# Kernel tuning notes

Measured on AMD Instinct MI355X. Metric: run time of the kernel, lower is better.

The kernel has to match this reference:

```python
import jax, jax.numpy as jnp
import numpy as np

N_NODES = 50000
N_EDGES = 800000
D_IN = 256
D_HID = 128


def setup_inputs() -> dict:
    key = jax.random.key(0)
    ks = jax.random.split(key, 10)
    x = jax.random.normal(ks[0], (N_NODES, D_IN), dtype=jnp.float32)
    edge_index = jax.random.randint(ks[1], (2, N_EDGES), 0, N_NODES, dtype=jnp.int64)
    # GCNConv params (glorot-ish init), 3 layers: 256->128, 128->128, 128->128
    def glorot(k, fan_in, fan_out):
        s = jnp.sqrt(6.0 / (fan_in + fan_out))
        return jax.random.uniform(k, (fan_in, fan_out), jnp.float32, -s, s)
    W0 = glorot(ks[2], D_IN, D_HID)
    b0 = jnp.zeros((D_HID,), jnp.float32)
    W1 = glorot(ks[3], D_HID, D_HID)
    b1 = jnp.zeros((D_HID,), jnp.float32)
    W2 = glorot(ks[4], D_HID, D_HID)
    b2 = jnp.zeros((D_HID,), jnp.float32)
    return {"x": x, "edge_index": edge_index, "W0": W0, "b0": b0,
            "W1": W1, "b1": b1, "W2": W2, "b2": b2}


def _gcn_conv(x, W, b, src, dst, deg_inv_sqrt, deg_inv):
    # PyG GCNConv: x' = D^{-1/2} (A + I) D^{-1/2} (x W) + b
    h = x @ W  # [N, d_out]
    norm = deg_inv_sqrt[src] * deg_inv_sqrt[dst]  # [E]
    msg = h[src] * norm[:, None]  # gather + scale, [E, d_out]
    agg = jax.ops.segment_sum(msg, dst, num_segments=x.shape[0])
    # self-loop contribution: norm = deg^{-1/2} * deg^{-1/2} = 1/deg
    return agg + h * deg_inv[:, None] + b


def reference(x, edge_index, W0, b0, W1, b1, W2, b2):
    src, dst = edge_index[0], edge_index[1]
    n = x.shape[0]
    # degree with self loops (computed on destination, source_to_target flow)
    deg = jax.ops.segment_sum(jnp.ones((src.shape[0],), x.dtype), dst,
                              num_segments=n) + 1.0
    deg_inv_sqrt = deg ** -0.5
    deg_inv = 1.0 / deg
    h = jax.nn.relu(_gcn_conv(x, W0, b0, src, dst, deg_inv_sqrt, deg_inv))
    h = jax.nn.relu(_gcn_conv(h, W1, b1, src, dst, deg_inv_sqrt, deg_inv))
    h = jax.nn.relu(_gcn_conv(h, W2, b2, src, dst, deg_inv_sqrt, deg_inv))
    return h
```

## Files before the change

### kernel.cpp

```cpp
#include <hip/hip_runtime.h>

#define N_NODES 50000
#define N_EDGES 800000
#define D_HID   128

typedef unsigned int uint;
typedef unsigned short ushort;
typedef __attribute__((ext_vector_type(8))) short short8;
typedef __attribute__((ext_vector_type(4))) float f32x4;

#define SCAN_NB ((N_NODES + 255) / 256)

__global__ void deg_count_k(const int* __restrict__ dst, int* __restrict__ cnt, int e) {
    int i = blockIdx.x * 256 + threadIdx.x;
    if (i < e) atomicAdd(&cnt[dst[i]], 1);
}

__global__ void bsum_k(const int* __restrict__ cnt, int* __restrict__ bsum, int n) {
    int i = blockIdx.x * 256 + threadIdx.x;
    int v = (i < n) ? cnt[i] : 0;
#pragma unroll
    for (int off = 32; off; off >>= 1) v += __shfl_down(v, off, 64);
    __shared__ int ws[4];
    int lane = threadIdx.x & 63, w = threadIdx.x >> 6;
    if (lane == 0) ws[w] = v;
    __syncthreads();
    if (threadIdx.x == 0) bsum[blockIdx.x] = ws[0] + ws[1] + ws[2] + ws[3];
}

__global__ void bscan_k(const int* __restrict__ bsum, int* __restrict__ boff,
                        int* __restrict__ row_ptr_end, int nb) {
    __shared__ int s[256];
    int t = threadIdx.x;
    int v = (t < nb) ? bsum[t] : 0;
    s[t] = v;
    __syncthreads();
    for (int off = 1; off < 256; off <<= 1) {
        int u = (t >= off) ? s[t - off] : 0;
        __syncthreads();
        s[t] += u;
        __syncthreads();
    }
    if (t < nb) boff[t] = s[t] - v;
    if (t == 255) *row_ptr_end = s[255];
}

__global__ void scan3_k(const int* __restrict__ cnt, const int* __restrict__ boff,
                        int* __restrict__ row_ptr, float* __restrict__ dis,
                        float* __restrict__ dinv, int* __restrict__ cursor, int n) {
    __shared__ int s[256];
    int i = blockIdx.x * 256 + threadIdx.x;
    int t = threadIdx.x;
    int v = (i < n) ? cnt[i] : 0;
    s[t] = v;
    __syncthreads();
    for (int off = 1; off < 256; off <<= 1) {
        int u = (t >= off) ? s[t - off] : 0;
        __syncthreads();
        s[t] += u;
        __syncthreads();
    }
    if (i < n) {
        row_ptr[i] = boff[blockIdx.x] + s[t] - v;
        float d = (float)v + 1.0f;
        dis[i]  = rsqrtf(d);
        dinv[i] = 1.0f / d;
        cursor[i] = 0;
    }
}

__global__ void scatter_k(const int* __restrict__ src, const int* __restrict__ dst,
                          const int* __restrict__ row_ptr, int* __restrict__ cursor,
                          int2* __restrict__ cew,
                          const float* __restrict__ dis, int e) {
    int i = blockIdx.x * 256 + threadIdx.x;
    if (i < e) {
        int s = src[i], d = dst[i];
        int pos = row_ptr[d] + atomicAdd(&cursor[d], 1);
        cew[pos] = make_int2(s, __float_as_int(dis[s]));
    }
}

__device__ inline ushort f2bf(float f) {
    unsigned u = __float_as_uint(f);
    unsigned rounding = 0x7fffu + ((u >> 16) & 1u);
    return (ushort)((u + rounding) >> 16);
}
__device__ inline float bf_lo(uint v) { return __uint_as_float(v << 16); }
__device__ inline float bf_hi(uint v) { return __uint_as_float(v & 0xffff0000u); }

__global__ void wtrans_all_k(const float* __restrict__ W0, const float* __restrict__ W1,
                             const float* __restrict__ W2, ushort* __restrict__ Wt0,
                             ushort* __restrict__ Wt1, ushort* __restrict__ Wt2) {
    int i = blockIdx.x * 256 + threadIdx.x;
    const float* W; ushort* Wt; int K, j;
    if (i < 32768)      { W = W0; Wt = Wt0; K = 256; j = i; }
    else if (i < 49152) { W = W1; Wt = Wt1; K = 128; j = i - 32768; }
    else                { W = W2; Wt = Wt2; K = 128; j = i - 49152; }
    int k = j >> 7, n = j & 127;
    Wt[(size_t)n * K + k] = f2bf(W[j]);
}

template<int K, bool AF32>
__global__ __launch_bounds__(256) void mfma_gemm_k(const void* __restrict__ Ap,
                                                   const ushort* __restrict__ Bt,
                                                   ushort* __restrict__ H,
                                                   int M) {
    int tid = threadIdx.x;
    int w   = tid >> 6;
    int l   = tid & 63;
    int row = blockIdx.x * 64 + w * 16 + (l & 15);
    int rc  = row < M ? row : M - 1;
    int kg  = (l >> 4) * 8;

    const ushort* A16 = (const ushort*)Ap;
    const float*  A32 = (const float*)Ap;

    f32x4 acc[8];
#pragma unroll
    for (int c = 0; c < 8; ++c) acc[c] = (f32x4){0.f, 0.f, 0.f, 0.f};

#pragma unroll
    for (int k0 = 0; k0 < K; k0 += 32) {
        short8 a;
        if (AF32) {
            const float* ap = &A32[(size_t)rc * K + k0 + kg];
            float4 f0 = *(const float4*)ap;
            float4 f1 = *(const float4*)(ap + 4);
            a[0] = (short)f2bf(f0.x); a[1] = (short)f2bf(f0.y);
            a[2] = (short)f2bf(f0.z); a[3] = (short)f2bf(f0.w);
            a[4] = (short)f2bf(f1.x); a[5] = (short)f2bf(f1.y);
            a[6] = (short)f2bf(f1.z); a[7] = (short)f2bf(f1.w);
        } else {
            a = *(const short8*)&A16[(size_t)rc * K + k0 + kg];
        }
#pragma unroll
        for (int c = 0; c < 8; ++c) {
            short8 b = *(const short8*)&Bt[(size_t)(c * 16 + (l & 15)) * K + k0 + kg];
            acc[c] = __builtin_amdgcn_mfma_f32_16x16x32_bf16(a, b, acc[c], 0, 0, 0);
        }
    }

    int r_base = blockIdx.x * 64 + w * 16 + (l >> 4) * 4;
    int colb   = l & 15;
#pragma unroll
    for (int c = 0; c < 8; ++c) {
#pragma unroll
        for (int j = 0; j < 4; ++j) {
            int r = r_base + j;
            if (r < M) H[(size_t)r * 128 + c * 16 + colb] = f2bf(acc[c][j]);
        }
    }
}

template<bool LAST>
__global__ __launch_bounds__(256) void aggregate_k(const ushort* __restrict__ hb,
                                                   const int* __restrict__ row_ptr,
                                                   const int2* __restrict__ cew,
                                                   const float* __restrict__ dis,
                                                   const float* __restrict__ dinv,
                                                   const float* __restrict__ bias,
                                                   ushort* __restrict__ act,
                                                   float* __restrict__ out, int n) {
    int node = blockIdx.x * 4 + (threadIdx.x >> 6);
    if (node >= n) return;
    int lane = threadIdx.x & 63;
    int g  = lane >> 4;
    int cl = lane & 15;
    const char* base = (const char*)hb + (cl << 4);

    float ax[8];
#pragma unroll
    for (int j = 0; j < 8; ++j) ax[j] = 0.f;

    int beg = row_ptr[node], end = row_ptr[node + 1];
    for (int e = beg; e < end; e += 16) {
        int s[4]; float wv[4];
#pragma unroll
        for (int q = 0; q < 4; ++q) {
            int idx = e + q * 4 + g;
            bool v  = idx < end;
            int2 p  = cew[v ? idx : (end - 1)];
            s[q]  = p.x;
            wv[q] = v ? __int_as_float(p.y) : 0.f;
        }
        uint4 u[4];
#pragma unroll
        for (int q = 0; q < 4; ++q)
            u[q] = *(const uint4*)(base + ((size_t)s[q] << 8));
#pragma unroll
        for (int q = 0; q < 4; ++q) {
            float ww = wv[q];
            ax[0] += ww * bf_lo(u[q].x); ax[1] += ww * bf_hi(u[q].x);
            ax[2] += ww * bf_lo(u[q].y); ax[3] += ww * bf_hi(u[q].y);
            ax[4] += ww * bf_lo(u[q].z); ax[5] += ww * bf_hi(u[q].z);
            ax[6] += ww * bf_lo(u[q].w); ax[7] += ww * bf_hi(u[q].w);
        }
    }
#pragma unroll
    for (int j = 0; j < 8; ++j) {
        ax[j] += __shfl_xor(ax[j], 16);
        ax[j] += __shfl_xor(ax[j], 32);
    }
    if (g == 0) {
        float dn = dis[node], di = dinv[node];
        uint4 un = *(const uint4*)(base + ((size_t)node << 8));
        float hs[8] = {bf_lo(un.x), bf_hi(un.x), bf_lo(un.y), bf_hi(un.y),
                       bf_lo(un.z), bf_hi(un.z), bf_lo(un.w), bf_hi(un.w)};
        int c0 = cl * 8;
        float4 bv0 = *(const float4*)&bias[c0];
        float4 bv1 = *(const float4*)&bias[c0 + 4];
        float bb[8] = {bv0.x, bv0.y, bv0.z, bv0.w, bv1.x, bv1.y, bv1.z, bv1.w};
        float o[8];
#pragma unroll
        for (int j = 0; j < 8; ++j)
            o[j] = fmaxf(ax[j] * dn + hs[j] * di + bb[j], 0.f);
        if (LAST) {
            *(float4*)&out[(size_t)node * D_HID + c0]     = make_float4(o[0], o[1], o[2], o[3]);
            *(float4*)&out[(size_t)node * D_HID + c0 + 4] = make_float4(o[4], o[5], o[6], o[7]);
        } else {
            uint4 p;
            p.x = (uint)f2bf(o[0]) | ((uint)f2bf(o[1]) << 16);
            p.y = (uint)f2bf(o[2]) | ((uint)f2bf(o[3]) << 16);
            p.z = (uint)f2bf(o[4]) | ((uint)f2bf(o[5]) << 16);
            p.w = (uint)f2bf(o[6]) | ((uint)f2bf(o[7]) << 16);
            *(uint4*)((char*)act + ((size_t)node << 8) + (cl << 4)) = p;
        }
    }
}

extern "C" void kernel_launch(void* const* d_in, const int* in_sizes, int n_in,
                              void* d_out, int out_size, void* d_ws, size_t ws_size,
                              hipStream_t stream) {
    const float* x  = (const float*)d_in[0];
    const int*   ei = (const int*)d_in[1];
    const float* W0 = (const float*)d_in[2];
    const float* b0 = (const float*)d_in[3];
    const float* W1 = (const float*)d_in[4];
    const float* b1 = (const float*)d_in[5];
    const float* W2 = (const float*)d_in[6];
    const float* b2 = (const float*)d_in[7];
    float* out = (float*)d_out;

    const int N = N_NODES, E = N_EDGES;
    const int* src = ei;
    const int* dst = ei + E;

    char* w = (char*)d_ws;
    size_t off = 0;
    auto alloc = [&](size_t bytes) {
        size_t o = off;
        off += (bytes + 255) & ~(size_t)255;
        return o;
    };
    int*    cnt    = (int*)(w + alloc((size_t)N * 4));
    int*    cursor = (int*)(w + alloc((size_t)N * 4));
    float*  dis    = (float*)(w + alloc((size_t)N * 4));
    float*  dinv   = (float*)(w + alloc((size_t)N * 4));
    int*    rp     = (int*)(w + alloc((size_t)(N + 1) * 4));
    int*    bsum   = (int*)(w + alloc((size_t)SCAN_NB * 4));
    int*    boff   = (int*)(w + alloc((size_t)SCAN_NB * 4));
    int2*   cew    = (int2*)(w + alloc((size_t)E * 8));
    ushort* hb     = (ushort*)(w + alloc((size_t)N * D_HID * 2));
    ushort* act    = (ushort*)(w + alloc((size_t)N * D_HID * 2));
    ushort* Wt0    = (ushort*)(w + alloc((size_t)128 * 256 * 2));
    ushort* Wt1    = (ushort*)(w + alloc((size_t)128 * 128 * 2));
    ushort* Wt2    = (ushort*)(w + alloc((size_t)128 * 128 * 2));
    (void)ws_size; (void)n_in; (void)in_sizes; (void)out_size;

    hipMemsetAsync(cnt, 0, (size_t)N * 4, stream);

    deg_count_k<<<(E + 255) / 256, 256, 0, stream>>>(dst, cnt, E);
    bsum_k<<<SCAN_NB, 256, 0, stream>>>(cnt, bsum, N);
    bscan_k<<<1, 256, 0, stream>>>(bsum, boff, rp + N, SCAN_NB);
    scan3_k<<<SCAN_NB, 256, 0, stream>>>(cnt, boff, rp, dis, dinv, cursor, N);
    scatter_k<<<(E + 255) / 256, 256, 0, stream>>>(src, dst, rp, cursor, cew, dis, E);

    wtrans_all_k<<<256, 256, 0, stream>>>(W0, W1, W2, Wt0, Wt1, Wt2);

    int gemm_grid = (N + 63) / 64;
    int agg_grid  = (N + 3) / 4;

    mfma_gemm_k<256, true><<<gemm_grid, 256, 0, stream>>>(x, Wt0, hb, N);
    aggregate_k<false><<<agg_grid, 256, 0, stream>>>(hb, rp, cew, dis, dinv, b0, act, out, N);
    mfma_gemm_k<128, false><<<gemm_grid, 256, 0, stream>>>(act, Wt1, hb, N);
    aggregate_k<false><<<agg_grid, 256, 0, stream>>>(hb, rp, cew, dis, dinv, b1, act, out, N);
    mfma_gemm_k<128, false><<<gemm_grid, 256, 0, stream>>>(act, Wt2, hb, N);
    aggregate_k<true><<<agg_grid, 256, 0, stream>>>(hb, rp, cew, dis, dinv, b2, act, out, N);
}
```

Baseline: 275.7 us.

## Persistent register-resident-B GEMM, sorted CSR rows, int column array

Rewrites the MFMA GEMM as a persistent grid-stride kernel. Each wave keeps its slice of the transposed weights in registers and prefetches the next A tile while computing the current one. The CSR edge array shrinks from (src, weight) pairs to plain source indices, and the weight is now gathered from dis in the aggregation. A new per-row sort kernel orders neighbour indices so that feature gathers have better locality. This adds an extra sort pass, a serial insertion sort for rows longer than 64, and an extra dependent gather per edge.

```diff
diff --git a/kernel.cpp b/kernel.cpp
--- a/kernel.cpp
+++ b/kernel.cpp
@@ -71,13 +71,40 @@
 
 __global__ void scatter_k(const int* __restrict__ src, const int* __restrict__ dst,
                           const int* __restrict__ row_ptr, int* __restrict__ cursor,
-                          int2* __restrict__ cew,
-                          const float* __restrict__ dis, int e) {
+                          int* __restrict__ col, int e) {
     int i = blockIdx.x * 256 + threadIdx.x;
     if (i < e) {
         int s = src[i], d = dst[i];
         int pos = row_ptr[d] + atomicAdd(&cursor[d], 1);
-        cew[pos] = make_int2(s, __float_as_int(dis[s]));
+        col[pos] = s;
+    }
+}
+
+__global__ __launch_bounds__(256) void sortrow_k(const int* __restrict__ rp,
+                                                 int* __restrict__ col, int n) {
+    int node = blockIdx.x * 4 + (threadIdx.x >> 6);
+    if (node >= n) return;
+    int lane = threadIdx.x & 63;
+    int beg = rp[node], end = rp[node + 1];
+    int len = end - beg;
+    if (len <= 1) return;
+    if (len <= 64) {
+        int v = (lane < len) ? col[beg + lane] : 0x7fffffff;
+        for (int k = 2; k <= 64; k <<= 1) {
+            for (int j = k >> 1; j > 0; j >>= 1) {
+                int other = __shfl_xor(v, j);
+                bool up    = (lane & k) == 0;
+                bool small = (lane & j) == 0;
+                v = (small == up) ? min(v, other) : max(v, other);
+            }
+        }
+        if (lane < len) col[beg + lane] = v;
+    } else if (lane == 0) {
+        for (int i = beg + 1; i < end; ++i) {
+            int key = col[i]; int j = i - 1;
+            while (j >= beg && col[j] > key) { col[j + 1] = col[j]; --j; }
+            col[j + 1] = key;
+        }
     }
 }
 
@@ -88,6 +115,14 @@
 }
 __device__ inline float bf_lo(uint v) { return __uint_as_float(v << 16); }
 __device__ inline float bf_hi(uint v) { return __uint_as_float(v & 0xffff0000u); }
+__device__ inline short8 cvt8(float4 f0, float4 f1) {
+    short8 r;
+    r[0] = (short)f2bf(f0.x); r[1] = (short)f2bf(f0.y);
+    r[2] = (short)f2bf(f0.z); r[3] = (short)f2bf(f0.w);
+    r[4] = (short)f2bf(f1.x); r[5] = (short)f2bf(f1.y);
+    r[6] = (short)f2bf(f1.z); r[7] = (short)f2bf(f1.w);
+    return r;
+}
 
 __global__ void wtrans_all_k(const float* __restrict__ W0, const float* __restrict__ W1,
                              const float* __restrict__ W2, ushort* __restrict__ Wt0,
@@ -102,61 +137,81 @@
 }
 
 template<int K, bool AF32>
-__global__ __launch_bounds__(256) void mfma_gemm_k(const void* __restrict__ Ap,
-                                                   const ushort* __restrict__ Bt,
-                                                   ushort* __restrict__ H,
-                                                   int M) {
+__global__ __launch_bounds__(256, 3) void mfma_gemm_k(const void* __restrict__ Ap,
+                                                      const ushort* __restrict__ Bt,
+                                                      ushort* __restrict__ H,
+                                                      int M, int ntiles) {
+    constexpr int T   = K / 32;
+    constexpr int NC  = (K == 128) ? 4 : 2;
+    constexpr int RPT = (K == 128) ? 32 : 16;
     int tid = threadIdx.x;
-    int w   = tid >> 6;
-    int l   = tid & 63;
-    int row = blockIdx.x * 64 + w * 16 + (l & 15);
-    int rc  = row < M ? row : M - 1;
-    int kg  = (l >> 4) * 8;
-
-    const ushort* A16 = (const ushort*)Ap;
-    const float*  A32 = (const float*)Ap;
-
-    f32x4 acc[8];
-#pragma unroll
-    for (int c = 0; c < 8; ++c) acc[c] = (f32x4){0.f, 0.f, 0.f, 0.f};
-
-#pragma unroll
-    for (int k0 = 0; k0 < K; k0 += 32) {
-        short8 a;
-        if (AF32) {
-            const float* ap = &A32[(size_t)rc * K + k0 + kg];
-            float4 f0 = *(const float4*)ap;
-            float4 f1 = *(const float4*)(ap + 4);
-            a[0] = (short)f2bf(f0.x); a[1] = (short)f2bf(f0.y);
-            a[2] = (short)f2bf(f0.z); a[3] = (short)f2bf(f0.w);
-            a[4] = (short)f2bf(f1.x); a[5] = (short)f2bf(f1.y);
-            a[6] = (short)f2bf(f1.z); a[7] = (short)f2bf(f1.w);
+    int w = tid >> 6, l = tid & 63;
+    int lr = l & 15, kg = (l >> 4) * 8;
+    int rIn   = (K == 128) ? (w >> 1) * 16 : 0;
+    int cBase = (K == 128) ? (w & 1) * 64 : w * 32;
+
+    short8 b[NC][T];
+#pragma unroll
+    for (int c = 0; c < NC; ++c)
+#pragma unroll
+        for (int t = 0; t < T; ++t)
+            b[c][t] = *(const short8*)&Bt[(size_t)(cBase + c * 16 + lr) * K + t * 32 + kg];
+
+    int tile = blockIdx.x;
+    if (tile >= ntiles) return;
+    const int G = gridDim.x;
+
+    auto loadA = [&](int tl, short8* dst) {
+        int rc = tl * RPT + rIn + lr; if (rc >= M) rc = M - 1;
+        if constexpr (AF32) {
+            const float* A32 = (const float*)Ap;
+#pragma unroll
+            for (int t = 0; t < T; ++t) {
+                float4 f0 = *(const float4*)&A32[(size_t)rc * K + t * 32 + kg];
+                float4 f1 = *(const float4*)&A32[(size_t)rc * K + t * 32 + kg + 4];
+                dst[t] = cvt8(f0, f1);
+            }
         } else {
-            a = *(const short8*)&A16[(size_t)rc * K + k0 + kg];
-        }
-#pragma unroll
-        for (int c = 0; c < 8; ++c) {
-            short8 b = *(const short8*)&Bt[(size_t)(c * 16 + (l & 15)) * K + k0 + kg];
-            acc[c] = __builtin_amdgcn_mfma_f32_16x16x32_bf16(a, b, acc[c], 0, 0, 0);
-        }
-    }
-
-    int r_base = blockIdx.x * 64 + w * 16 + (l >> 4) * 4;
-    int colb   = l & 15;
-#pragma unroll
-    for (int c = 0; c < 8; ++c) {
-#pragma unroll
-        for (int j = 0; j < 4; ++j) {
-            int r = r_base + j;
-            if (r < M) H[(size_t)r * 128 + c * 16 + colb] = f2bf(acc[c][j]);
-        }
+            const ushort* A16 = (const ushort*)Ap;
+#pragma unroll
+            for (int t = 0; t < T; ++t)
+                dst[t] = *(const short8*)&A16[(size_t)rc * K + t * 32 + kg];
+        }
+    };
+
+    short8 a[T];
+    loadA(tile, a);
+    for (; tile < ntiles; tile += G) {
+        short8 an[T];
+        int nt = tile + G;
+        if (nt < ntiles) loadA(nt, an);
+
+        f32x4 acc[NC];
+#pragma unroll
+        for (int c = 0; c < NC; ++c) acc[c] = (f32x4){0.f, 0.f, 0.f, 0.f};
+#pragma unroll
+        for (int t = 0; t < T; ++t)
+#pragma unroll
+            for (int c = 0; c < NC; ++c)
+                acc[c] = __builtin_amdgcn_mfma_f32_16x16x32_bf16(a[t], b[c][t], acc[c], 0, 0, 0);
+
+        int rs = tile * RPT + rIn + (l >> 4) * 4;
+#pragma unroll
+        for (int c = 0; c < NC; ++c)
+#pragma unroll
+            for (int j = 0; j < 4; ++j) {
+                int r = rs + j;
+                if (r < M) H[(size_t)r * 128 + cBase + c * 16 + lr] = f2bf(acc[c][j]);
+            }
+#pragma unroll
+        for (int t = 0; t < T; ++t) a[t] = an[t];
     }
 }
 
 template<bool LAST>
 __global__ __launch_bounds__(256) void aggregate_k(const ushort* __restrict__ hb,
                                                    const int* __restrict__ row_ptr,
-                                                   const int2* __restrict__ cew,
+                                                   const int* __restrict__ col,
                                                    const float* __restrict__ dis,
                                                    const float* __restrict__ dinv,
                                                    const float* __restrict__ bias,
@@ -180,9 +235,8 @@
         for (int q = 0; q < 4; ++q) {
             int idx = e + q * 4 + g;
             bool v  = idx < end;
-            int2 p  = cew[v ? idx : (end - 1)];
-            s[q]  = p.x;
-            wv[q] = v ? __int_as_float(p.y) : 0.f;
+            s[q]  = col[v ? idx : (end - 1)];
+            wv[q] = v ? dis[s[q]] : 0.f;
         }
         uint4 u[4];
 #pragma unroll
@@ -260,7 +314,7 @@
     int*    rp     = (int*)(w + alloc((size_t)(N + 1) * 4));
     int*    bsum   = (int*)(w + alloc((size_t)SCAN_NB * 4));
     int*    boff   = (int*)(w + alloc((size_t)SCAN_NB * 4));
-    int2*   cew    = (int2*)(w + alloc((size_t)E * 8));
+    int*    col    = (int*)(w + alloc((size_t)E * 4));
     ushort* hb     = (ushort*)(w + alloc((size_t)N * D_HID * 2));
     ushort* act    = (ushort*)(w + alloc((size_t)N * D_HID * 2));
     ushort* Wt0    = (ushort*)(w + alloc((size_t)128 * 256 * 2));
@@ -274,17 +328,20 @@
     bsum_k<<<SCAN_NB, 256, 0, stream>>>(cnt, bsum, N);
     bscan_k<<<1, 256, 0, stream>>>(bsum, boff, rp + N, SCAN_NB);
     scan3_k<<<SCAN_NB, 256, 0, stream>>>(cnt, boff, rp, dis, dinv, cursor, N);
-    scatter_k<<<(E + 255) / 256, 256, 0, stream>>>(src, dst, rp, cursor, cew, dis, E);
+    scatter_k<<<(E + 255) / 256, 256, 0, stream>>>(src, dst, rp, cursor, col, E);
+    sortrow_k<<<(N + 3) / 4, 256, 0, stream>>>(rp, col, N);
 
     wtrans_all_k<<<256, 256, 0, stream>>>(W0, W1, W2, Wt0, Wt1, Wt2);
 
-    int gemm_grid = (N + 63) / 64;
-    int agg_grid  = (N + 3) / 4;
-
-    mfma_gemm_k<256, true><<<gemm_grid, 256, 0, stream>>>(x, Wt0, hb, N);
-    aggregate_k<false><<<agg_grid, 256, 0, stream>>>(hb, rp, cew, dis, dinv, b0, act, out, N);
-    mfma_gemm_k<128, false><<<gemm_grid, 256, 0, stream>>>(act, Wt1, hb, N);
-    aggregate_k<false><<<agg_grid, 256, 0, stream>>>(hb, rp, cew, dis, dinv, b1, act, out, N);
-    mfma_gemm_k<128, false><<<gemm_grid, 256, 0, stream>>>(act, Wt2, hb, N);
-    aggregate_k<true><<<agg_grid, 256, 0, stream>>>(hb, rp, cew, dis, dinv, b2, act, out, N);
-}
+    const int GG = 768;
+    int nt256 = (N + 15) / 16;
+    int nt128 = (N + 31) / 32;
+    int agg_grid = (N + 3) / 4;
+
+    mfma_gemm_k<256, true><<<GG, 256, 0, stream>>>(x, Wt0, hb, N, nt256);
+    aggregate_k<false><<<agg_grid, 256, 0, stream>>>(hb, rp, col, dis, dinv, b0, act, out, N);
+    mfma_gemm_k<128, false><<<GG, 256, 0, stream>>>(act, Wt1, hb, N, nt128);
+    aggregate_k<false><<<agg_grid, 256, 0, stream>>>(hb, rp, col, dis, dinv, b1, act, out, N);
+    mfma_gemm_k<128, false><<<GG, 256, 0, stream>>>(act, Wt2, hb, N, nt128);
+    aggregate_k<true><<<agg_grid, 256, 0, stream>>>(hb, rp, col, dis, dinv, b2, act, out, N);
+}
```

Measured after the change: 291.9 us. 1.06x slower.
